# Kernel optimization log

Measured on AMD Instinct MI355X. Metric: run time of the kernel, lower is better.

The kernel has to match this reference:

```python
import jax, jax.numpy as jnp
import numpy as np
from jax import lax

B, H, W, C = 8, 640, 640, 3


def setup_inputs() -> dict:
    key = jax.random.key(0)
    ks = jax.random.split(key, 10)
    def rn(k, shape, scale=0.05):
        return jax.random.normal(k, shape, dtype=jnp.float32) * scale
    return {
        "x": jax.random.normal(ks[0], (B, H, W, C), dtype=jnp.float32),
        "conv1_k": rn(ks[1], (5, 5, C, 32)),
        "conv1_b": jnp.zeros((32,), jnp.float32),
        "conv2_k": rn(ks[2], (5, 5, 32, 32)),
        "conv2_b": jnp.zeros((32,), jnp.float32),
        "d1_k": rn(ks[3], (32, 300)),
        "d1_b": jnp.zeros((300,), jnp.float32),
        "d2_k": rn(ks[4], (300, 1340)),
        "d2_b": jnp.zeros((1340,), jnp.float32),
        "w1_k": rn(ks[5], (2001,)),
        "w1_b": jnp.zeros((2001,), jnp.float32),
        "w2_k": rn(ks[6], (801,)),
        "w2_b": jnp.zeros((801,), jnp.float32),
        "w3_k": rn(ks[7], (321,)),
        "w3_b": jnp.zeros((321,), jnp.float32),
        "w4_k": rn(ks[8], (65,)),
        "w4_b": jnp.zeros((65,), jnp.float32),
    }


def _conv_relu(x, k, b):
    y = lax.conv_general_dilated(x, k, window_strides=(1, 1), padding='SAME',
                                 dimension_numbers=('NHWC', 'HWIO', 'NHWC'))
    return jax.nn.relu(y + b)


def _maxpool(x, stride):
    # pool_size=(2,2), given strides, padding='same' (TF semantics ~ SAME here)
    return lax.reduce_window(x, -jnp.inf, lax.max,
                             (1, 2, 2, 1), (1, stride, stride, 1), 'SAME')


def _head(chans, n_rows, k, b):
    # original: reshape slice to (n_rows, -1); per row, Dense(input_dim=1)
    # on the row reshaped to (-1,1), then keep only row index 1 of the result
    # => relu(row_elem_1 * k + b). Vectorized over all rows at once.
    s = chans.reshape(n_rows, -1)[:, 1]            # (n_rows,)
    return jax.nn.relu(s[:, None] * k[None, :] + b[None, :]).reshape(-1)


def _forward(x, conv1_k, conv1_b, conv2_k, conv2_b, d1_k, d1_b, d2_k, d2_b,
             w1_k, w1_b, w2_k, w2_b, w3_k, w3_b, w4_k, w4_b):
    y = _maxpool(_conv_relu(x, conv1_k, conv1_b), 4)      # (B,H/4,W/4,32)
    y = _maxpool(_conv_relu(y, conv2_k, conv2_b), 2)      # (B,H/8,W/8,32)
    y = jax.nn.relu(jnp.einsum('bhwc,cd->bhwd', y, d1_k) + d1_b)   # (...,300)
    y = jax.nn.relu(jnp.einsum('bhwc,cd->bhwd', y, d2_k) + d2_b)   # (...,1340)
    o1 = _head(y[..., :160], 32, w1_k, w1_b)     # 32*2001
    o2 = _head(y[..., 160:320], 32, w2_k, w2_b)  # 32*801
    o3 = _head(y[..., 320:480], 32, w3_k, w3_b)  # 32*321
    o4 = _head(y[..., 480:510], 6, w4_k, w4_b)   # 6*65
    return jnp.concatenate([o1, o2, o3, o4], axis=0)  # (100326,)


def reference(x, conv1_k, conv1_b, conv2_k, conv2_b, d1_k, d1_b, d2_k, d2_b,
              w1_k, w1_b, w2_k, w2_b, w3_k, w3_b, w4_k, w4_b):
    return _forward(x, conv1_k, conv1_b, conv2_k, conv2_b, d1_k, d1_b,
                    d2_k, d2_b, w1_k, w1_b, w2_k, w2_b, w3_k, w3_b, w4_k, w4_b)
```

## Files before the change

kernel.cpp:

```cpp
#include <hip/hip_runtime.h>

#define TPB 512

__device__ __forceinline__ float frelu(float v) { return v > 0.f ? v : 0.f; }

__global__ __launch_bounds__(TPB, 1) void hyper_kernel(
    const float* __restrict__ x,
    const float* __restrict__ k1,
    const float* __restrict__ b1,
    const float* __restrict__ k2,
    const float* __restrict__ b2,
    const float* __restrict__ d1k,
    const float* __restrict__ d1b,
    const float* __restrict__ d2k,
    const float* __restrict__ d2b,
    const float* __restrict__ w1k, const float* __restrict__ w1b,
    const float* __restrict__ w2k, const float* __restrict__ w2b,
    const float* __restrict__ w3k, const float* __restrict__ w3b,
    const float* __restrict__ w4k, const float* __restrict__ w4b,
    float* __restrict__ out)
{
    __shared__ float xs[26 * 26 * 3];
    __shared__ float k1s[2400];
    __shared__ float p1[36 * 32];
    __shared__ float part[32 * 132];
    __shared__ float zz[32];
    __shared__ float aa[300];
    __shared__ float d2cols[3 * 300];
    __shared__ float d1bs[300];
    __shared__ float b1s[32];
    __shared__ float b2s[32];
    __shared__ float d2bs[3];
    __shared__ float yy[3];

    const int p   = blockIdx.x;
    const int tid = threadIdx.x;

    int b, h2, w2, nch, ch0, ch1, ch2;
    if (p < 32) {
        b = p >> 2; h2 = (p & 3) * 20; w2 = 0;
        nch = 3; ch0 = 1; ch1 = 161; ch2 = 321;
    } else {
        const int qb[6] = {0, 1, 2, 4, 5, 6};
        const int qh[6] = {0, 26, 53, 0, 26, 53};
        const int qw[6] = {0, 53, 26, 0, 53, 26};
        const int qc[6] = {481, 491, 501, 481, 491, 501};
        const int q = p - 32;
        b = qb[q]; h2 = qh[q]; w2 = qw[q];
        nch = 1; ch0 = qc[q]; ch1 = 0; ch2 = 0;
    }

    float rd1[32];
    if (tid < 300) {
#pragma unroll
        for (int c = 0; c < 32; ++c) rd1[c] = d1k[c * 300 + tid];
    }

    float hk1[4], hb1[4], hk2[2], hb2[2], hk3 = 0.f, hb3 = 0.f, hk4 = 0.f, hb4 = 0.f;
    if (p < 32) {
#pragma unroll
        for (int u = 0; u < 4; ++u) {
            const int i = tid + u * TPB;
            if (i < 2001) { hk1[u] = w1k[i]; hb1[u] = w1b[i]; }
        }
#pragma unroll
        for (int u = 0; u < 2; ++u) {
            const int i = tid + u * TPB;
            if (i < 801) { hk2[u] = w2k[i]; hb2[u] = w2b[i]; }
        }
        if (tid < 321) { hk3 = w3k[tid]; hb3 = w3b[tid]; }
    } else {
        if (tid < 65) { hk4 = w4k[tid]; hb4 = w4b[tid]; }
    }

    const int r0 = 8 * h2 - 10;
    const int c0 = 8 * w2 - 10;
    for (int idx = tid; idx < 26 * 26 * 3; idx += TPB) {
        const int ic = idx % 3;
        const int rest = idx / 3;
        const int row = rest / 26, col = rest % 26;
        const int gh = r0 + row, gw = c0 + col;
        float v = 0.f;
        if ((unsigned)gh < 640u && (unsigned)gw < 640u)
            v = x[((b * 640 + gh) * 640 + gw) * 3 + ic];
        xs[idx] = v;
    }
    for (int i = tid; i < 2400; i += TPB) k1s[i] = k1[i];
    for (int t = tid; t < nch * 300; t += TPB) {
        const int wv = t / 300, j = t - wv * 300;
        const int ch = (wv == 0) ? ch0 : ((wv == 1) ? ch1 : ch2);
        d2cols[wv * 300 + j] = d2k[j * 1340 + ch];
    }
    for (int i = tid; i < 300; i += TPB) d1bs[i] = d1b[i];
    if (tid < 32) { b1s[tid] = b1[tid]; b2s[tid] = b2[tid]; }
    if (tid < nch) {
        const int ch = (tid == 0) ? ch0 : ((tid == 1) ? ch1 : ch2);
        d2bs[tid] = d2b[ch];
    }
    __syncthreads();

    if (tid < 288) {
        const int pos = tid >> 3;
        const int ocg = tid & 7;
        const int hp6 = pos / 6, wp6 = pos % 6;
        const int hp = 2 * h2 - 2 + hp6;
        const int wp = 2 * w2 - 2 + wp6;
        float r00 = 0.f, r01 = 0.f, r10 = 0.f, r11 = 0.f;
        float acc[4][4];
        const bool ok = ((unsigned)hp < 160u && (unsigned)wp < 160u);
        if (ok) {
            const float bias0 = b1s[ocg * 4 + 0];
            const float bias1 = b1s[ocg * 4 + 1];
            const float bias2 = b1s[ocg * 4 + 2];
            const float bias3 = b1s[ocg * 4 + 3];
#pragma unroll
            for (int t4 = 0; t4 < 4; ++t4) {
                acc[t4][0] = bias0; acc[t4][1] = bias1;
                acc[t4][2] = bias2; acc[t4][3] = bias3;
            }
            const int rbase = 4 * hp6, cbase = 4 * wp6;
            for (int dh = 0; dh < 5; ++dh)
                for (int dw = 0; dw < 5; ++dw) {
#pragma unroll
                    for (int ic = 0; ic < 3; ++ic) {
                        const float4 kv = *(const float4*)&k1s[(((dh * 5 + dw) * 3 + ic) << 5) + (ocg << 2)];
                        const float* xp = &xs[((rbase + dh) * 26 + cbase + dw) * 3 + ic];
                        const float x00 = xp[0];
                        const float x01 = xp[3];
                        const float x10 = xp[78];
                        const float x11 = xp[81];
                        acc[0][0] += x00 * kv.x; acc[0][1] += x00 * kv.y;
                        acc[0][2] += x00 * kv.z; acc[0][3] += x00 * kv.w;
                        acc[1][0] += x01 * kv.x; acc[1][1] += x01 * kv.y;
                        acc[1][2] += x01 * kv.z; acc[1][3] += x01 * kv.w;
                        acc[2][0] += x10 * kv.x; acc[2][1] += x10 * kv.y;
                        acc[2][2] += x10 * kv.z; acc[2][3] += x10 * kv.w;
                        acc[3][0] += x11 * kv.x; acc[3][1] += x11 * kv.y;
                        acc[3][2] += x11 * kv.z; acc[3][3] += x11 * kv.w;
                    }
                }
            r00 = frelu(fmaxf(fmaxf(acc[0][0], acc[1][0]), fmaxf(acc[2][0], acc[3][0])));
            r01 = frelu(fmaxf(fmaxf(acc[0][1], acc[1][1]), fmaxf(acc[2][1], acc[3][1])));
            r10 = frelu(fmaxf(fmaxf(acc[0][2], acc[1][2]), fmaxf(acc[2][2], acc[3][2])));
            r11 = frelu(fmaxf(fmaxf(acc[0][3], acc[1][3]), fmaxf(acc[2][3], acc[3][3])));
        }
        float* pp = &p1[pos * 32 + ocg * 4];
        pp[0] = r00; pp[1] = r01; pp[2] = r10; pp[3] = r11;
    }
    __syncthreads();

    if (tid < 256) {
        const int ic  = tid >> 3;
        const int ocg = tid & 7;
        float acc[4][4];
#pragma unroll
        for (int q = 0; q < 4; ++q) { acc[q][0] = acc[q][1] = acc[q][2] = acc[q][3] = 0.f; }
        const float4* k2v = (const float4*)(k2 + ic * 32 + ocg * 4);
#pragma unroll
        for (int dh = 0; dh < 5; ++dh)
#pragma unroll
            for (int dw = 0; dw < 5; ++dw) {
                const int tap = dh * 5 + dw;
                const float4 kv = k2v[tap * 256];
                float pv[4];
#pragma unroll
                for (int pos = 0; pos < 4; ++pos) {
                    const int dy = pos >> 1, dx = pos & 1;
                    pv[pos] = p1[((dy + dh) * 6 + (dx + dw)) * 32 + ic];
                }
#pragma unroll
                for (int pos = 0; pos < 4; ++pos) {
                    acc[pos][0] += pv[pos] * kv.x;
                    acc[pos][1] += pv[pos] * kv.y;
                    acc[pos][2] += pv[pos] * kv.z;
                    acc[pos][3] += pv[pos] * kv.w;
                }
            }
#pragma unroll
        for (int pos = 0; pos < 4; ++pos)
#pragma unroll
            for (int o = 0; o < 4; ++o)
                part[ic * 132 + pos * 32 + ocg * 4 + o] = acc[pos][o];
    }
    __syncthreads();

    if (tid < 128) {
        const int oc  = tid >> 2;
        const int pos = tid & 3;
        float s = b2s[oc];
        for (int ic = 0; ic < 32; ++ic)
            s += part[ic * 132 + pos * 32 + oc];
        float v = frelu(s);
        v = fmaxf(v, __shfl_xor(v, 1));
        v = fmaxf(v, __shfl_xor(v, 2));
        if (pos == 0) zz[oc] = v;
    }
    __syncthreads();

    if (tid < 300) {
        float acc = d1bs[tid];
#pragma unroll
        for (int c = 0; c < 32; ++c)
            acc += zz[c] * rd1[c];
        aa[tid] = frelu(acc);
    }
    __syncthreads();

    if (tid < 64 * nch) {
        const int wv = tid >> 6, lane = tid & 63;
        float s = 0.f;
        for (int j = lane; j < 300; j += 64)
            s += aa[j] * d2cols[wv * 300 + j];
        for (int off = 32; off > 0; off >>= 1)
            s += __shfl_down(s, off);
        if (lane == 0) yy[wv] = frelu(s + d2bs[wv]);
    }
    __syncthreads();

    if (p < 32) {
        const float y1 = yy[0], y2 = yy[1], y3 = yy[2];
#pragma unroll
        for (int u = 0; u < 4; ++u) {
            const int i = tid + u * TPB;
            if (i < 2001) out[p * 2001 + i] = frelu(y1 * hk1[u] + hb1[u]);
        }
#pragma unroll
        for (int u = 0; u < 2; ++u) {
            const int i = tid + u * TPB;
            if (i < 801) out[64032 + p * 801 + i] = frelu(y2 * hk2[u] + hb2[u]);
        }
        if (tid < 321) out[89664 + p * 321 + tid] = frelu(y3 * hk3 + hb3);
    } else {
        const float y4 = yy[0];
        if (tid < 65) out[99936 + (p - 32) * 65 + tid] = frelu(y4 * hk4 + hb4);
    }
}

extern "C" void kernel_launch(void* const* d_in, const int* in_sizes, int n_in,
                              void* d_out, int out_size, void* d_ws, size_t ws_size,
                              hipStream_t stream) {
    (void)in_sizes; (void)n_in; (void)d_ws; (void)ws_size; (void)out_size;
    const float* x   = (const float*)d_in[0];
    const float* k1  = (const float*)d_in[1];
    const float* b1  = (const float*)d_in[2];
    const float* k2  = (const float*)d_in[3];
    const float* b2  = (const float*)d_in[4];
    const float* d1k = (const float*)d_in[5];
    const float* d1b = (const float*)d_in[6];
    const float* d2k = (const float*)d_in[7];
    const float* d2b = (const float*)d_in[8];
    const float* w1k = (const float*)d_in[9];
    const float* w1b = (const float*)d_in[10];
    const float* w2k = (const float*)d_in[11];
    const float* w2b = (const float*)d_in[12];
    const float* w3k = (const float*)d_in[13];
    const float* w3b = (const float*)d_in[14];
    const float* w4k = (const float*)d_in[15];
    const float* w4b = (const float*)d_in[16];

    hyper_kernel<<<38, TPB, 0, stream>>>(
        x, k1, b1, k2, b2, d1k, d1b, d2k, d2b,
        w1k, w1b, w2k, w2b, w3k, w3b, w4k, w4b,
        (float*)d_out);
}
```

Before: 16.37 us.

## Prefetch biases and weights into registers, use planar input tile for conv1

Biases, d2 columns and conv2 weights are now loaded from global memory straight into registers at kernel start instead of being staged through shared memory. This lets the conv2 weight loads, done by threads 256-511, overlap with the input tile load. The input tile is stored channel-planar, so conv1 reads each row once with float2 loads and reuses it across the five horizontal taps. conv2 now runs on threads 256-511, which raises register pressure (25 float4 weights per thread) and risks spills under the 512-thread launch bound.

New measurement: 14.87 us. 1.1x faster.

```diff
diff --git a/kernel.cpp b/kernel.cpp
--- a/kernel.cpp
+++ b/kernel.cpp
@@ -20,17 +20,12 @@
     const float* __restrict__ w4k, const float* __restrict__ w4b,
     float* __restrict__ out)
 {
-    __shared__ float xs[26 * 26 * 3];
+    __shared__ float xs[3 * 676];
     __shared__ float k1s[2400];
     __shared__ float p1[36 * 32];
     __shared__ float part[32 * 132];
     __shared__ float zz[32];
     __shared__ float aa[300];
-    __shared__ float d2cols[3 * 300];
-    __shared__ float d1bs[300];
-    __shared__ float b1s[32];
-    __shared__ float b2s[32];
-    __shared__ float d2bs[3];
     __shared__ float yy[3];
 
     const int p   = blockIdx.x;
@@ -51,9 +46,39 @@
     }
 
     float rd1[32];
+    float d1breg = 0.f;
     if (tid < 300) {
 #pragma unroll
         for (int c = 0; c < 32; ++c) rd1[c] = d1k[c * 300 + tid];
+        d1breg = d1b[tid];
+    }
+
+    float4 b1reg = make_float4(0.f, 0.f, 0.f, 0.f);
+    if (tid < 288) b1reg = *(const float4*)&b1[(tid & 7) * 4];
+
+    float b2reg = (tid < 128) ? b2[tid >> 2] : 0.f;
+
+    float d2reg[5] = {0.f, 0.f, 0.f, 0.f, 0.f};
+    float d2breg = 0.f;
+    if (tid < 192) {
+        const int wv = tid >> 6;
+        if (wv < nch) {
+            const int ch = (wv == 0) ? ch0 : ((wv == 1) ? ch1 : ch2);
+#pragma unroll
+            for (int u = 0; u < 5; ++u) {
+                const int j = (tid & 63) + 64 * u;
+                if (j < 300) d2reg[u] = d2k[j * 1340 + ch];
+            }
+            d2breg = d2b[ch];
+        }
+    }
+
+    float4 kreg[25];
+    if (tid >= 256) {
+        const int t = tid - 256;
+        const float4* k2v = (const float4*)k2 + (t >> 3) * 8 + (t & 7);
+#pragma unroll
+        for (int tap = 0; tap < 25; ++tap) kreg[tap] = k2v[tap * 256];
     }
 
     float hk1[4], hb1[4], hk2[2], hb2[2], hk3 = 0.f, hb3 = 0.f, hk4 = 0.f, hb4 = 0.f;
@@ -75,10 +100,10 @@
 
     const int r0 = 8 * h2 - 10;
     const int c0 = 8 * w2 - 10;
-    for (int idx = tid; idx < 26 * 26 * 3; idx += TPB) {
-        const int ic = idx % 3;
-        const int rest = idx / 3;
-        const int row = rest / 26, col = rest % 26;
+    for (int idx = tid; idx < 3 * 676; idx += TPB) {
+        const int ic  = idx / 676;
+        const int rem = idx - ic * 676;
+        const int row = rem / 26, col = rem - (rem / 26) * 26;
         const int gh = r0 + row, gw = c0 + col;
         float v = 0.f;
         if ((unsigned)gh < 640u && (unsigned)gw < 640u)
@@ -86,49 +111,41 @@
         xs[idx] = v;
     }
     for (int i = tid; i < 2400; i += TPB) k1s[i] = k1[i];
-    for (int t = tid; t < nch * 300; t += TPB) {
-        const int wv = t / 300, j = t - wv * 300;
-        const int ch = (wv == 0) ? ch0 : ((wv == 1) ? ch1 : ch2);
-        d2cols[wv * 300 + j] = d2k[j * 1340 + ch];
-    }
-    for (int i = tid; i < 300; i += TPB) d1bs[i] = d1b[i];
-    if (tid < 32) { b1s[tid] = b1[tid]; b2s[tid] = b2[tid]; }
-    if (tid < nch) {
-        const int ch = (tid == 0) ? ch0 : ((tid == 1) ? ch1 : ch2);
-        d2bs[tid] = d2b[ch];
-    }
     __syncthreads();
 
     if (tid < 288) {
         const int pos = tid >> 3;
         const int ocg = tid & 7;
-        const int hp6 = pos / 6, wp6 = pos % 6;
+        const int hp6 = pos / 6, wp6 = pos - hp6 * 6;
         const int hp = 2 * h2 - 2 + hp6;
         const int wp = 2 * w2 - 2 + wp6;
         float r00 = 0.f, r01 = 0.f, r10 = 0.f, r11 = 0.f;
-        float acc[4][4];
-        const bool ok = ((unsigned)hp < 160u && (unsigned)wp < 160u);
-        if (ok) {
-            const float bias0 = b1s[ocg * 4 + 0];
-            const float bias1 = b1s[ocg * 4 + 1];
-            const float bias2 = b1s[ocg * 4 + 2];
-            const float bias3 = b1s[ocg * 4 + 3];
+        if ((unsigned)hp < 160u && (unsigned)wp < 160u) {
+            float acc[4][4];
 #pragma unroll
             for (int t4 = 0; t4 < 4; ++t4) {
-                acc[t4][0] = bias0; acc[t4][1] = bias1;
-                acc[t4][2] = bias2; acc[t4][3] = bias3;
+                acc[t4][0] = b1reg.x; acc[t4][1] = b1reg.y;
+                acc[t4][2] = b1reg.z; acc[t4][3] = b1reg.w;
             }
             const int rbase = 4 * hp6, cbase = 4 * wp6;
-            for (int dh = 0; dh < 5; ++dh)
-                for (int dw = 0; dw < 5; ++dw) {
-#pragma unroll
-                    for (int ic = 0; ic < 3; ++ic) {
+#pragma unroll
+            for (int dh = 0; dh < 5; ++dh) {
+#pragma unroll
+                for (int ic = 0; ic < 3; ++ic) {
+                    const float* rp0 = &xs[ic * 676 + (rbase + dh) * 26 + cbase];
+                    const float2 a0 = *(const float2*)(rp0);
+                    const float2 a2 = *(const float2*)(rp0 + 2);
+                    const float2 a4 = *(const float2*)(rp0 + 4);
+                    const float2 c0_ = *(const float2*)(rp0 + 26);
+                    const float2 c2_ = *(const float2*)(rp0 + 28);
+                    const float2 c4_ = *(const float2*)(rp0 + 30);
+                    const float xr0[6] = {a0.x, a0.y, a2.x, a2.y, a4.x, a4.y};
+                    const float xr1[6] = {c0_.x, c0_.y, c2_.x, c2_.y, c4_.x, c4_.y};
+#pragma unroll
+                    for (int dw = 0; dw < 5; ++dw) {
                         const float4 kv = *(const float4*)&k1s[(((dh * 5 + dw) * 3 + ic) << 5) + (ocg << 2)];
-                        const float* xp = &xs[((rbase + dh) * 26 + cbase + dw) * 3 + ic];
-                        const float x00 = xp[0];
-                        const float x01 = xp[3];
-                        const float x10 = xp[78];
-                        const float x11 = xp[81];
+                        const float x00 = xr0[dw], x01 = xr0[dw + 1];
+                        const float x10 = xr1[dw], x11 = xr1[dw + 1];
                         acc[0][0] += x00 * kv.x; acc[0][1] += x00 * kv.y;
                         acc[0][2] += x00 * kv.z; acc[0][3] += x00 * kv.w;
                         acc[1][0] += x01 * kv.x; acc[1][1] += x01 * kv.y;
@@ -139,29 +156,28 @@
                         acc[3][2] += x11 * kv.z; acc[3][3] += x11 * kv.w;
                     }
                 }
+            }
             r00 = frelu(fmaxf(fmaxf(acc[0][0], acc[1][0]), fmaxf(acc[2][0], acc[3][0])));
             r01 = frelu(fmaxf(fmaxf(acc[0][1], acc[1][1]), fmaxf(acc[2][1], acc[3][1])));
             r10 = frelu(fmaxf(fmaxf(acc[0][2], acc[1][2]), fmaxf(acc[2][2], acc[3][2])));
             r11 = frelu(fmaxf(fmaxf(acc[0][3], acc[1][3]), fmaxf(acc[2][3], acc[3][3])));
         }
-        float* pp = &p1[pos * 32 + ocg * 4];
-        pp[0] = r00; pp[1] = r01; pp[2] = r10; pp[3] = r11;
-    }
-    __syncthreads();
-
-    if (tid < 256) {
-        const int ic  = tid >> 3;
-        const int ocg = tid & 7;
+        *(float4*)&p1[pos * 32 + ocg * 4] = make_float4(r00, r01, r10, r11);
+    }
+    __syncthreads();
+
+    if (tid >= 256) {
+        const int t   = tid - 256;
+        const int ic  = t >> 3;
+        const int ocg = t & 7;
         float acc[4][4];
 #pragma unroll
         for (int q = 0; q < 4; ++q) { acc[q][0] = acc[q][1] = acc[q][2] = acc[q][3] = 0.f; }
-        const float4* k2v = (const float4*)(k2 + ic * 32 + ocg * 4);
 #pragma unroll
         for (int dh = 0; dh < 5; ++dh)
 #pragma unroll
             for (int dw = 0; dw < 5; ++dw) {
-                const int tap = dh * 5 + dw;
-                const float4 kv = k2v[tap * 256];
+                const float4 kv = kreg[dh * 5 + dw];
                 float pv[4];
 #pragma unroll
                 for (int pos = 0; pos < 4; ++pos) {
@@ -187,7 +203,7 @@
     if (tid < 128) {
         const int oc  = tid >> 2;
         const int pos = tid & 3;
-        float s = b2s[oc];
+        float s = b2reg;
         for (int ic = 0; ic < 32; ++ic)
             s += part[ic * 132 + pos * 32 + oc];
         float v = frelu(s);
@@ -198,7 +214,7 @@
     __syncthreads();
 
     if (tid < 300) {
-        float acc = d1bs[tid];
+        float acc = d1breg;
 #pragma unroll
         for (int c = 0; c < 32; ++c)
             acc += zz[c] * rd1[c];
@@ -209,11 +225,14 @@
     if (tid < 64 * nch) {
         const int wv = tid >> 6, lane = tid & 63;
         float s = 0.f;
-        for (int j = lane; j < 300; j += 64)
-            s += aa[j] * d2cols[wv * 300 + j];
+#pragma unroll
+        for (int u = 0; u < 5; ++u) {
+            const int j = lane + 64 * u;
+            if (j < 300) s += aa[j] * d2reg[u];
+        }
         for (int off = 32; off > 0; off >>= 1)
             s += __shfl_down(s, off);
-        if (lane == 0) yy[wv] = frelu(s + d2bs[wv]);
+        if (lane == 0) yy[wv] = frelu(s + d2breg);
     }
     __syncthreads();
 
```
